# Performance work log

Measured on AMD Instinct MI355X. Metric: run time of the kernel, lower is better.

The kernel has to match this reference:

```python
import jax, jax.numpy as jnp
import numpy as np

K, A, DIM = 1024, 16384, 512


def setup_inputs() -> dict:
    key = jax.random.key(0)
    ks = jax.random.split(key, 8)
    B, H, W = 2048, 8, 8
    z_t = jax.random.randint(ks[0], (B, H, W), 0, K, dtype=jnp.int64)
    z_tp1 = jax.random.randint(ks[1], (B, H, W), 0, K, dtype=jnp.int64)
    embed_w = jax.random.normal(ks[2], (K, DIM), dtype=jnp.float32) * 0.02
    # MLP: Linear(2*dim -> dim), GELU, Linear(dim -> dim)
    lim1 = 1.0 / np.sqrt(2 * DIM)
    w1 = jax.random.uniform(ks[3], (2 * DIM, DIM), minval=-lim1, maxval=lim1, dtype=jnp.float32)
    b1 = jax.random.uniform(ks[4], (DIM,), minval=-lim1, maxval=lim1, dtype=jnp.float32)
    lim2 = 1.0 / np.sqrt(DIM)
    w2 = jax.random.uniform(ks[5], (DIM, DIM), minval=-lim2, maxval=lim2, dtype=jnp.float32)
    b2 = jax.random.uniform(ks[6], (DIM,), minval=-lim2, maxval=lim2, dtype=jnp.float32)
    codebook_w = jax.random.normal(ks[7], (A, DIM), dtype=jnp.float32) * 0.02
    return {"z_t": z_t, "z_tp1": z_tp1, "embed_w": embed_w, "w1": w1, "b1": b1,
            "w2": w2, "b2": b2, "codebook_w": codebook_w}


def reference(z_t, z_tp1, embed_w, w1, b1, w2, b2, codebook_w):
    B = z_t.shape[0]
    # embed int code grids and mean-pool over H*W tokens -> [B, dim]
    e_t = embed_w[z_t.reshape(B, -1)].mean(axis=1)
    e_tp1 = embed_w[z_tp1.reshape(B, -1)].mean(axis=1)
    h = jnp.concatenate([e_t, e_tp1], axis=-1)          # [B, 2*dim]
    h = jax.nn.gelu(h @ w1 + b1, approximate=False)
    e = h @ w2 + b2                                      # [B, dim]
    # VQ: squared L2 distance to each code, argmin, gather
    d2 = (jnp.sum(e * e, axis=1, keepdims=True)
          - 2.0 * e @ codebook_w.T
          + jnp.sum(codebook_w * codebook_w, axis=1)[None, :])  # [B, A]
    ids = jnp.argmin(d2, axis=1)                         # [B]
    q = codebook_w[ids]                                  # [B, dim]
    return ids, q
```

## Files before the change

### kernel.cpp

```cpp
#include <hip/hip_runtime.h>
#include <hip/hip_bf16.h>

#define TOK 64
#define DIMC 512

typedef __attribute__((ext_vector_type(8))) short v8s;
typedef __attribute__((ext_vector_type(4))) float v4f;

__device__ __forceinline__ unsigned int f2ord(float f) {
  unsigned int u = __float_as_uint(f);
  return (u & 0x80000000u) ? ~u : (u | 0x80000000u);
}

__device__ __forceinline__ float gelu_exact(float x) {
  return 0.5f * x * (1.0f + erff(x * 0.70710678118654752440f));
}

__device__ __forceinline__ unsigned short f2bf(float x) {
  unsigned int u = __float_as_uint(x);
  return (unsigned short)((u + 0x7FFFu + ((u >> 16) & 1u)) >> 16);
}
__device__ __forceinline__ float bf2f(unsigned short h) {
  return __uint_as_float((unsigned int)h << 16);
}

__device__ __forceinline__ void gl2lds16(const void* g, void* l) {
  __builtin_amdgcn_global_load_lds((const __attribute__((address_space(1))) void*)g,
                                   (__attribute__((address_space(3))) void*)l,
                                   16, 0, 0);
}

__global__ __launch_bounds__(256) void k_prep(
    const int* __restrict__ zt, const int* __restrict__ ztp,
    const float* __restrict__ emb,
    unsigned short* __restrict__ hh, unsigned short* __restrict__ hl,
    unsigned long long* __restrict__ rowmin,
    const float* __restrict__ w1, unsigned short* __restrict__ w1th,
    unsigned short* __restrict__ w1tl,
    const float* __restrict__ w2, unsigned short* __restrict__ w2th,
    unsigned short* __restrict__ w2tl,
    const float* __restrict__ cb, unsigned short* __restrict__ ch,
    unsigned short* __restrict__ cl, float* __restrict__ cnorm) {
  __shared__ int codes[128];
  __shared__ float tbuf[32][33];
  const int bid = blockIdx.x;
  const int tid = threadIdx.x;

  if (bid < 2048) {
    const int b = bid;
    if (tid < 64) codes[tid] = zt[b * TOK + tid];
    else if (tid < 128) codes[tid] = ztp[b * TOK + (tid - 64)];
    if (tid == 0) rowmin[b] = 0xFFFFFFFFFFFFFFFFull;
    __syncthreads();
    const int half = tid >> 7;
    const int c4 = tid & 127;
    const float4* emb4 = (const float4*)emb;
    float4 s = make_float4(0.f, 0.f, 0.f, 0.f);
    #pragma unroll 8
    for (int t = 0; t < TOK; t++) {
      const int code = codes[half * TOK + t];
      const float4 v = emb4[code * 128 + c4];
      s.x += v.x; s.y += v.y; s.z += v.z; s.w += v.w;
    }
    const float inv = 1.0f / 64.0f;
    float f[4] = {s.x * inv, s.y * inv, s.z * inv, s.w * inv};
    unsigned short hi[4], lo[4];
    #pragma unroll
    for (int i = 0; i < 4; i++) {
      hi[i] = f2bf(f[i]);
      lo[i] = f2bf(f[i] - bf2f(hi[i]));
    }
    const int off = b * 1024 + half * 512 + c4 * 4;
    *(ushort4*)&hh[off] = make_ushort4(hi[0], hi[1], hi[2], hi[3]);
    *(ushort4*)&hl[off] = make_ushort4(lo[0], lo[1], lo[2], lo[3]);
  } else if (bid < 2816) {
    const float* w; unsigned short *wth, *wtl; int Kd, N, k0, n0;
    if (bid < 2560) {
      const int i = bid - 2048;
      w = w1; wth = w1th; wtl = w1tl; Kd = 1024; N = 512;
      k0 = (i & 31) * 32; n0 = (i >> 5) * 32;
    } else {
      const int i = bid - 2560;
      w = w2; wth = w2th; wtl = w2tl; Kd = 512; N = 512;
      k0 = (i & 15) * 32; n0 = (i >> 4) * 32;
    }
    const int c = tid & 31, r = tid >> 5;
    #pragma unroll
    for (int i = 0; i < 4; i++)
      tbuf[r + i * 8][c] = w[(size_t)(k0 + r + i * 8) * N + n0 + c];
    __syncthreads();
    #pragma unroll
    for (int i = 0; i < 4; i++) {
      const float v = tbuf[c][r + i * 8];
      const unsigned short hi = f2bf(v);
      const unsigned short lo = f2bf(v - bf2f(hi));
      wth[(size_t)(n0 + r + i * 8) * Kd + k0 + c] = hi;
      wtl[(size_t)(n0 + r + i * 8) * Kd + k0 + c] = lo;
    }
  } else {
    const int row = (bid - 2816) * 4 + (tid >> 6);
    const int lane = tid & 63;
    const float4* cb4 = (const float4*)cb;
    const float4 va = cb4[row * 128 + lane * 2];
    const float4 vb = cb4[row * 128 + lane * 2 + 1];
    float s = va.x * va.x + va.y * va.y + va.z * va.z + va.w * va.w
            + vb.x * vb.x + vb.y * vb.y + vb.z * vb.z + vb.w * vb.w;
    float f[8] = {va.x, va.y, va.z, va.w, vb.x, vb.y, vb.z, vb.w};
    unsigned short hi[8], lo[8];
    #pragma unroll
    for (int i = 0; i < 8; i++) {
      hi[i] = f2bf(f[i]);
      lo[i] = f2bf(f[i] - bf2f(hi[i]));
    }
    ushort4* chp = (ushort4*)&ch[row * DIMC + lane * 8];
    ushort4* clp = (ushort4*)&cl[row * DIMC + lane * 8];
    chp[0] = make_ushort4(hi[0], hi[1], hi[2], hi[3]);
    chp[1] = make_ushort4(hi[4], hi[5], hi[6], hi[7]);
    clp[0] = make_ushort4(lo[0], lo[1], lo[2], lo[3]);
    clp[1] = make_ushort4(lo[4], lo[5], lo[6], lo[7]);
    #pragma unroll
    for (int off = 32; off > 0; off >>= 1) s += __shfl_down(s, off);
    if (lane == 0) cnorm[row] = s;
  }
}

template <bool GELU>
__global__ __launch_bounds__(256) void k_gemm(const unsigned short* __restrict__ Ah_,
                                              const unsigned short* __restrict__ Al_,
                                              const unsigned short* __restrict__ Bh_,
                                              const unsigned short* __restrict__ Bl_,
                                              const float* __restrict__ bias,
                                              unsigned short* __restrict__ oh,
                                              unsigned short* __restrict__ ol,
                                              int Kd, int N) {
  __shared__ unsigned short AhS[2][32 * 32];
  __shared__ unsigned short AlS[2][32 * 32];
  __shared__ unsigned short BhS[2][64 * 32];
  __shared__ unsigned short BlS[2][64 * 32];

  const int tid = threadIdx.x;
  const int lane = tid & 63;
  const int wid = tid >> 6;
  const int m0 = blockIdx.x * 32;
  const int n0 = blockIdx.y * 64;

  const unsigned short* Ab_h = Ah_ + (size_t)m0 * Kd;
  const unsigned short* Ab_l = Al_ + (size_t)m0 * Kd;
  const unsigned short* Bb_h = Bh_ + (size_t)n0 * Kd;
  const unsigned short* Bb_l = Bl_ + (size_t)n0 * Kd;

  const int srow = lane >> 2;
  const int sk = (lane & 3) * 8;
  const int wm = wid >> 1, wn = wid & 1;
  const int fr = lane & 15;
  const int fq = (lane >> 4) * 8;

  v4f acc[2];
  acc[0] = (v4f)(0.f);
  acc[1] = (v4f)(0.f);

  auto stage = [&](int b, int k0) {
    #pragma unroll
    for (int u = 0; u < 3; u++) {
      const int i = wid * 3 + u;
      const unsigned short* gs; unsigned short* ls; int rbase;
      if (i < 2)      { gs = Ab_h; ls = AhS[b]; rbase = i * 16; }
      else if (i < 4) { gs = Ab_l; ls = AlS[b]; rbase = (i - 2) * 16; }
      else if (i < 8) { gs = Bb_h; ls = BhS[b]; rbase = (i - 4) * 16; }
      else            { gs = Bb_l; ls = BlS[b]; rbase = (i - 8) * 16; }
      gl2lds16(gs + (size_t)(rbase + srow) * Kd + k0 + sk, ls + rbase * 32);
    }
  };

  stage(0, 0);
  int cur = 0;
  for (int k0 = 0; k0 < Kd; k0 += 32) {
    __syncthreads();
    if (k0 + 32 < Kd) stage(cur ^ 1, k0 + 32);

    const int ar = (wm * 16 + fr) * 32 + fq;
    const v8s ah = *(const v8s*)&AhS[cur][ar];
    const v8s al = *(const v8s*)&AlS[cur][ar];
    #pragma unroll
    for (int nt = 0; nt < 2; nt++) {
      const int br = (wn * 32 + nt * 16 + fr) * 32 + fq;
      const v8s bh = *(const v8s*)&BhS[cur][br];
      const v8s bl = *(const v8s*)&BlS[cur][br];
      acc[nt] = __builtin_amdgcn_mfma_f32_16x16x32_bf16(ah, bh, acc[nt], 0, 0, 0);
      acc[nt] = __builtin_amdgcn_mfma_f32_16x16x32_bf16(ah, bl, acc[nt], 0, 0, 0);
      acc[nt] = __builtin_amdgcn_mfma_f32_16x16x32_bf16(al, bh, acc[nt], 0, 0, 0);
    }
    cur ^= 1;
  }

  const int col16 = lane & 15;
  const int q = lane >> 4;
  #pragma unroll
  for (int nt = 0; nt < 2; nt++) {
    const int col = n0 + wn * 32 + nt * 16 + col16;
    const float bv = bias[col];
    #pragma unroll
    for (int reg = 0; reg < 4; reg++) {
      const int row = m0 + wm * 16 + q * 4 + reg;
      float v = acc[nt][reg] + bv;
      if (GELU) v = gelu_exact(v);
      const unsigned short hi = f2bf(v);
      oh[(size_t)row * N + col] = hi;
      ol[(size_t)row * N + col] = f2bf(v - bf2f(hi));
    }
  }
}

__global__ __launch_bounds__(256, 2) void k_vq(const unsigned short* __restrict__ eh,
                                               const unsigned short* __restrict__ el,
                                               const unsigned short* __restrict__ ch,
                                               const unsigned short* __restrict__ cl,
                                               const float* __restrict__ cnorm,
                                               unsigned long long* __restrict__ rowmin) {
  __shared__ unsigned short Ah[128 * 32];
  __shared__ unsigned short Al[128 * 32];
  __shared__ unsigned short Bh[256 * 32];
  __shared__ unsigned short Bl[256 * 32];

  const int tid = threadIdx.x;
  const int lane = tid & 63;
  const int wid = tid >> 6;
  const int bid = blockIdx.x;
  const int j = bid >> 3;
  const int x = j & 15;
  const int y = ((j >> 4) << 3) | (bid & 7);
  const int r0 = x * 128;
  const int c0 = y * 256;

  v4f acc[4][8];
  #pragma unroll
  for (int i = 0; i < 4; i++)
    #pragma unroll
    for (int jj = 0; jj < 8; jj++) acc[i][jj] = (v4f)(0.f);

  const unsigned short* ehB = eh + (size_t)r0 * DIMC;
  const unsigned short* elB = el + (size_t)r0 * DIMC;
  const unsigned short* chB = ch + (size_t)c0 * DIMC;
  const unsigned short* clB = cl + (size_t)c0 * DIMC;

  const int srow = lane >> 2;
  const int sk = (lane & 3) * 8;
  const int wm = wid >> 1;
  const int wn = wid & 1;
  const int fr = lane & 15;
  const int fq = (lane >> 4) * 8;

  for (int k0 = 0; k0 < DIMC; k0 += 32) {
    __syncthreads();
    #pragma unroll
    for (int u = 0; u < 12; u++) {
      const int i = wid * 12 + u;
      const unsigned short* gs; unsigned short* ls; int rbase;
      if (i < 8)       { gs = ehB; ls = Ah; rbase = i * 16; }
      else if (i < 16) { gs = elB; ls = Al; rbase = (i - 8) * 16; }
      else if (i < 32) { gs = chB; ls = Bh; rbase = (i - 16) * 16; }
      else             { gs = clB; ls = Bl; rbase = (i - 32) * 16; }
      gl2lds16(gs + (size_t)(rbase + srow) * DIMC + k0 + sk, ls + rbase * 32);
    }
    __syncthreads();

    v8s ahf[4], alf[4];
    #pragma unroll
    for (int mt = 0; mt < 4; mt++) {
      const int ar = (wm * 64 + mt * 16 + fr) * 32 + fq;
      ahf[mt] = *(const v8s*)&Ah[ar];
      alf[mt] = *(const v8s*)&Al[ar];
    }
    #pragma unroll
    for (int nt = 0; nt < 8; nt++) {
      const int br = (wn * 128 + nt * 16 + fr) * 32 + fq;
      const v8s bhf = *(const v8s*)&Bh[br];
      const v8s blf = *(const v8s*)&Bl[br];
      #pragma unroll
      for (int mt = 0; mt < 4; mt++) {
        acc[mt][nt] = __builtin_amdgcn_mfma_f32_16x16x32_bf16(ahf[mt], bhf, acc[mt][nt], 0, 0, 0);
        acc[mt][nt] = __builtin_amdgcn_mfma_f32_16x16x32_bf16(ahf[mt], blf, acc[mt][nt], 0, 0, 0);
        acc[mt][nt] = __builtin_amdgcn_mfma_f32_16x16x32_bf16(alf[mt], bhf, acc[mt][nt], 0, 0, 0);
      }
    }
  }

  const int col16 = lane & 15;
  const int q = lane >> 4;
  float cn[8];
  #pragma unroll
  for (int nt = 0; nt < 8; nt++) cn[nt] = cnorm[c0 + wn * 128 + nt * 16 + col16];

  #pragma unroll
  for (int mt = 0; mt < 4; mt++) {
    #pragma unroll
    for (int reg = 0; reg < 4; reg++) {
      const int row = r0 + wm * 64 + mt * 16 + q * 4 + reg;
      float best = fmaf(-2.f, acc[mt][0][reg], cn[0]);
      int bid2 = c0 + wn * 128 + col16;
      #pragma unroll
      for (int nt = 1; nt < 8; nt++) {
        const float s = fmaf(-2.f, acc[mt][nt][reg], cn[nt]);
        const int id = c0 + wn * 128 + nt * 16 + col16;
        if (s < best) { best = s; bid2 = id; }
      }
      unsigned long long v =
          ((unsigned long long)f2ord(best) << 32) | (unsigned int)bid2;
      #pragma unroll
      for (int off = 8; off > 0; off >>= 1) {
        const unsigned long long o = __shfl_down(v, off, 16);
        if (o < v) v = o;
      }
      if (col16 == 0) atomicMin(&rowmin[row], v);
    }
  }
}

__global__ __launch_bounds__(64) void k_final(const unsigned long long* __restrict__ rowmin,
                                              const float* __restrict__ cb,
                                              float* __restrict__ out,
                                              int B) {
  const int b = blockIdx.x;
  const int t = threadIdx.x;
  const unsigned long long m = rowmin[b];
  const int id = (int)(unsigned int)(m & 0xFFFFFFFFull);
  if (t == 0) out[b] = (float)id;
  float4* q4 = (float4*)(out + B) + b * 128;
  const float4* cb4 = (const float4*)cb + (size_t)id * 128;
  q4[t] = cb4[t];
  q4[t + 64] = cb4[t + 64];
}

extern "C" void kernel_launch(void* const* d_in, const int* in_sizes, int n_in,
                              void* d_out, int out_size, void* d_ws, size_t ws_size,
                              hipStream_t stream) {
  const int* zt = (const int*)d_in[0];
  const int* ztp = (const int*)d_in[1];
  const float* emb = (const float*)d_in[2];
  const float* w1 = (const float*)d_in[3];
  const float* b1 = (const float*)d_in[4];
  const float* w2 = (const float*)d_in[5];
  const float* b2 = (const float*)d_in[6];
  const float* cb = (const float*)d_in[7];
  float* out = (float*)d_out;

  const int B = in_sizes[0] / TOK;
  const int A = in_sizes[7] / DIMC;

  char* p = (char*)d_ws;
  unsigned short* hh = (unsigned short*)p;  p += (size_t)B * 1024 * 2;
  unsigned short* hl = (unsigned short*)p;  p += (size_t)B * 1024 * 2;
  unsigned short* w1th = (unsigned short*)p; p += (size_t)512 * 1024 * 2;
  unsigned short* w1tl = (unsigned short*)p; p += (size_t)512 * 1024 * 2;
  unsigned short* w2th = (unsigned short*)p; p += (size_t)512 * 512 * 2;
  unsigned short* w2tl = (unsigned short*)p; p += (size_t)512 * 512 * 2;
  unsigned short* h1h = (unsigned short*)p; p += (size_t)B * DIMC * 2;
  unsigned short* h1l = (unsigned short*)p; p += (size_t)B * DIMC * 2;
  unsigned short* eh = (unsigned short*)p;  p += (size_t)B * DIMC * 2;
  unsigned short* el = (unsigned short*)p;  p += (size_t)B * DIMC * 2;
  unsigned short* ch = (unsigned short*)p;  p += (size_t)A * DIMC * 2;
  unsigned short* cl = (unsigned short*)p;  p += (size_t)A * DIMC * 2;
  float* cnorm = (float*)p;                 p += (size_t)A * 4;
  unsigned long long* rowmin = (unsigned long long*)p;

  k_prep<<<2816 + A / 4, 256, 0, stream>>>(zt, ztp, emb, hh, hl, rowmin,
                                           w1, w1th, w1tl, w2, w2th, w2tl,
                                           cb, ch, cl, cnorm);
  k_gemm<true><<<dim3(B / 32, 512 / 64), 256, 0, stream>>>(hh, hl, w1th, w1tl, b1, h1h, h1l, 1024, 512);
  k_gemm<false><<<dim3(B / 32, 512 / 64), 256, 0, stream>>>(h1h, h1l, w2th, w2tl, b2, eh, el, 512, 512);
  k_vq<<<(B / 128) * (A / 256), 256, 0, stream>>>(eh, el, ch, cl, cnorm, rowmin);
  k_final<<<B, 64, 0, stream>>>(rowmin, cb, out, B);
}
```

Baseline: 234.6 us.

## Switch VQ distance GEMM to 32x32x16 MFMA tiles and split launch in two

The VQ kernel now uses 32x32x16 bf16 MFMA instructions with 16-float accumulators instead of 16x16x32, halving the number of fragment loads from LDS per k-step and changing the epilogue row mapping and shuffle reduction to 32-lane groups. The single 1024-block launch is split into two 512-block launches offset by a column-tile base parameter. The larger MFMA shape aims for better LDS-to-MFMA ratio; splitting the launch adds a launch boundary and may reduce tail overlap.

```diff
diff --git a/kernel.cpp b/kernel.cpp
--- a/kernel.cpp
+++ b/kernel.cpp
@@ -6,6 +6,7 @@
 
 typedef __attribute__((ext_vector_type(8))) short v8s;
 typedef __attribute__((ext_vector_type(4))) float v4f;
+typedef __attribute__((ext_vector_type(16))) float v16f;
 
 __device__ __forceinline__ unsigned int f2ord(float f) {
   unsigned int u = __float_as_uint(f);
@@ -216,7 +217,8 @@
                                                const unsigned short* __restrict__ ch,
                                                const unsigned short* __restrict__ cl,
                                                const float* __restrict__ cnorm,
-                                               unsigned long long* __restrict__ rowmin) {
+                                               unsigned long long* __restrict__ rowmin,
+                                               int y0) {
   __shared__ unsigned short Ah[128 * 32];
   __shared__ unsigned short Al[128 * 32];
   __shared__ unsigned short Bh[256 * 32];
@@ -228,15 +230,15 @@
   const int bid = blockIdx.x;
   const int j = bid >> 3;
   const int x = j & 15;
-  const int y = ((j >> 4) << 3) | (bid & 7);
+  const int y = y0 + (((j >> 4) << 3) | (bid & 7));
   const int r0 = x * 128;
   const int c0 = y * 256;
 
-  v4f acc[4][8];
+  v16f acc[2][4];
   #pragma unroll
-  for (int i = 0; i < 4; i++)
-    #pragma unroll
-    for (int jj = 0; jj < 8; jj++) acc[i][jj] = (v4f)(0.f);
+  for (int i = 0; i < 2; i++)
+    #pragma unroll
+    for (int jj = 0; jj < 4; jj++) acc[i][jj] = (v16f)(0.f);
 
   const unsigned short* ehB = eh + (size_t)r0 * DIMC;
   const unsigned short* elB = el + (size_t)r0 * DIMC;
@@ -247,8 +249,8 @@
   const int sk = (lane & 3) * 8;
   const int wm = wid >> 1;
   const int wn = wid & 1;
-  const int fr = lane & 15;
-  const int fq = (lane >> 4) * 8;
+  const int col32 = lane & 31;
+  const int khalf = lane >> 5;
 
   for (int k0 = 0; k0 < DIMC; k0 += 32) {
     __syncthreads();
@@ -264,54 +266,56 @@
     }
     __syncthreads();
 
-    v8s ahf[4], alf[4];
-    #pragma unroll
-    for (int mt = 0; mt < 4; mt++) {
-      const int ar = (wm * 64 + mt * 16 + fr) * 32 + fq;
-      ahf[mt] = *(const v8s*)&Ah[ar];
-      alf[mt] = *(const v8s*)&Al[ar];
-    }
-    #pragma unroll
-    for (int nt = 0; nt < 8; nt++) {
-      const int br = (wn * 128 + nt * 16 + fr) * 32 + fq;
-      const v8s bhf = *(const v8s*)&Bh[br];
-      const v8s blf = *(const v8s*)&Bl[br];
+    #pragma unroll
+    for (int sub = 0; sub < 2; sub++) {
+      const int ko = sub * 16 + khalf * 8;
+      v8s ahf[2], alf[2];
       #pragma unroll
-      for (int mt = 0; mt < 4; mt++) {
-        acc[mt][nt] = __builtin_amdgcn_mfma_f32_16x16x32_bf16(ahf[mt], bhf, acc[mt][nt], 0, 0, 0);
-        acc[mt][nt] = __builtin_amdgcn_mfma_f32_16x16x32_bf16(ahf[mt], blf, acc[mt][nt], 0, 0, 0);
-        acc[mt][nt] = __builtin_amdgcn_mfma_f32_16x16x32_bf16(alf[mt], bhf, acc[mt][nt], 0, 0, 0);
+      for (int mt = 0; mt < 2; mt++) {
+        const int ar = (wm * 64 + mt * 32 + col32) * 32 + ko;
+        ahf[mt] = *(const v8s*)&Ah[ar];
+        alf[mt] = *(const v8s*)&Al[ar];
       }
-    }
-  }
-
-  const int col16 = lane & 15;
-  const int q = lane >> 4;
-  float cn[8];
+      #pragma unroll
+      for (int nt = 0; nt < 4; nt++) {
+        const int br = (wn * 128 + nt * 32 + col32) * 32 + ko;
+        const v8s bhf = *(const v8s*)&Bh[br];
+        const v8s blf = *(const v8s*)&Bl[br];
+        #pragma unroll
+        for (int mt = 0; mt < 2; mt++) {
+          acc[mt][nt] = __builtin_amdgcn_mfma_f32_32x32x16_bf16(ahf[mt], bhf, acc[mt][nt], 0, 0, 0);
+          acc[mt][nt] = __builtin_amdgcn_mfma_f32_32x32x16_bf16(ahf[mt], blf, acc[mt][nt], 0, 0, 0);
+          acc[mt][nt] = __builtin_amdgcn_mfma_f32_32x32x16_bf16(alf[mt], bhf, acc[mt][nt], 0, 0, 0);
+        }
+      }
+    }
+  }
+
+  float cn[4];
   #pragma unroll
-  for (int nt = 0; nt < 8; nt++) cn[nt] = cnorm[c0 + wn * 128 + nt * 16 + col16];
+  for (int nt = 0; nt < 4; nt++) cn[nt] = cnorm[c0 + wn * 128 + nt * 32 + col32];
 
   #pragma unroll
-  for (int mt = 0; mt < 4; mt++) {
-    #pragma unroll
-    for (int reg = 0; reg < 4; reg++) {
-      const int row = r0 + wm * 64 + mt * 16 + q * 4 + reg;
+  for (int mt = 0; mt < 2; mt++) {
+    #pragma unroll
+    for (int reg = 0; reg < 16; reg++) {
+      const int row = r0 + wm * 64 + mt * 32 + (reg & 3) + 8 * (reg >> 2) + 4 * khalf;
       float best = fmaf(-2.f, acc[mt][0][reg], cn[0]);
-      int bid2 = c0 + wn * 128 + col16;
+      int bid2 = c0 + wn * 128 + col32;
       #pragma unroll
-      for (int nt = 1; nt < 8; nt++) {
+      for (int nt = 1; nt < 4; nt++) {
         const float s = fmaf(-2.f, acc[mt][nt][reg], cn[nt]);
-        const int id = c0 + wn * 128 + nt * 16 + col16;
+        const int id = c0 + wn * 128 + nt * 32 + col32;
         if (s < best) { best = s; bid2 = id; }
       }
       unsigned long long v =
           ((unsigned long long)f2ord(best) << 32) | (unsigned int)bid2;
       #pragma unroll
-      for (int off = 8; off > 0; off >>= 1) {
-        const unsigned long long o = __shfl_down(v, off, 16);
+      for (int off = 16; off > 0; off >>= 1) {
+        const unsigned long long o = __shfl_down(v, off, 32);
         if (o < v) v = o;
       }
-      if (col16 == 0) atomicMin(&rowmin[row], v);
+      if (col32 == 0) atomicMin(&rowmin[row], v);
     }
   }
 }
@@ -368,6 +372,7 @@
                                            cb, ch, cl, cnorm);
   k_gemm<true><<<dim3(B / 32, 512 / 64), 256, 0, stream>>>(hh, hl, w1th, w1tl, b1, h1h, h1l, 1024, 512);
   k_gemm<false><<<dim3(B / 32, 512 / 64), 256, 0, stream>>>(h1h, h1l, w2th, w2tl, b2, eh, el, 512, 512);
-  k_vq<<<(B / 128) * (A / 256), 256, 0, stream>>>(eh, el, ch, cl, cnorm, rowmin);
+  k_vq<<<512, 256, 0, stream>>>(eh, el, ch, cl, cnorm, rowmin, 0);
+  k_vq<<<512, 256, 0, stream>>>(eh, el, ch, cl, cnorm, rowmin, 32);
   k_final<<<B, 64, 0, stream>>>(rowmin, cb, out, B);
 }
```

Result: slower. 257.3 us (+9.7%).

## Double-buffer VQ GEMM LDS tiles and shrink codebook tile to 128

Applied to the files above, without the earlier changes.

Splits the VQ distance kernel's shared-memory tiles into two buffers so that the global-to-LDS loads for the next K-slice are issued while MFMAs run on the current one, with one barrier per iteration. The codebook tile per block drops from 256 to 128 columns, halving the accumulators and doubling the grid. This aims to hide load latency and ease register pressure. The cost is lower data reuse per block, twice as many per-row atomicMin reductions, and more LDS per block.

```diff
diff --git a/kernel.cpp b/kernel.cpp
--- a/kernel.cpp
+++ b/kernel.cpp
@@ -29,6 +29,7 @@
                                    (__attribute__((address_space(3))) void*)l,
                                    16, 0, 0);
 }
+
 
 __global__ __launch_bounds__(256) void k_prep(
     const int* __restrict__ zt, const int* __restrict__ ztp,
@@ -217,10 +218,10 @@
                                                const unsigned short* __restrict__ cl,
                                                const float* __restrict__ cnorm,
                                                unsigned long long* __restrict__ rowmin) {
-  __shared__ unsigned short Ah[128 * 32];
-  __shared__ unsigned short Al[128 * 32];
-  __shared__ unsigned short Bh[256 * 32];
-  __shared__ unsigned short Bl[256 * 32];
+  __shared__ unsigned short AhS[2][128 * 32];
+  __shared__ unsigned short AlS[2][128 * 32];
+  __shared__ unsigned short BhS[2][128 * 32];
+  __shared__ unsigned short BlS[2][128 * 32];
 
   const int tid = threadIdx.x;
   const int lane = tid & 63;
@@ -230,13 +231,13 @@
   const int x = j & 15;
   const int y = ((j >> 4) << 3) | (bid & 7);
   const int r0 = x * 128;
-  const int c0 = y * 256;
-
-  v4f acc[4][8];
+  const int c0 = y * 128;
+
+  v4f acc[4][4];
   #pragma unroll
   for (int i = 0; i < 4; i++)
     #pragma unroll
-    for (int jj = 0; jj < 8; jj++) acc[i][jj] = (v4f)(0.f);
+    for (int jj = 0; jj < 4; jj++) acc[i][jj] = (v4f)(0.f);
 
   const unsigned short* ehB = eh + (size_t)r0 * DIMC;
   const unsigned short* elB = el + (size_t)r0 * DIMC;
@@ -250,32 +251,37 @@
   const int fr = lane & 15;
   const int fq = (lane >> 4) * 8;
 
+  auto stage = [&](int b, int k0) {
+    #pragma unroll
+    for (int u = 0; u < 8; u++) {
+      const int i = wid * 8 + u;
+      const unsigned short* gs; unsigned short* ls; int rbase;
+      if (i < 8)       { gs = ehB; ls = AhS[b]; rbase = i * 16; }
+      else if (i < 16) { gs = elB; ls = AlS[b]; rbase = (i - 8) * 16; }
+      else if (i < 24) { gs = chB; ls = BhS[b]; rbase = (i - 16) * 16; }
+      else             { gs = clB; ls = BlS[b]; rbase = (i - 24) * 16; }
+      gl2lds16(gs + (size_t)(rbase + srow) * DIMC + k0 + sk, ls + rbase * 32);
+    }
+  };
+
+  stage(0, 0);
+  int cur = 0;
   for (int k0 = 0; k0 < DIMC; k0 += 32) {
     __syncthreads();
-    #pragma unroll
-    for (int u = 0; u < 12; u++) {
-      const int i = wid * 12 + u;
-      const unsigned short* gs; unsigned short* ls; int rbase;
-      if (i < 8)       { gs = ehB; ls = Ah; rbase = i * 16; }
-      else if (i < 16) { gs = elB; ls = Al; rbase = (i - 8) * 16; }
-      else if (i < 32) { gs = chB; ls = Bh; rbase = (i - 16) * 16; }
-      else             { gs = clB; ls = Bl; rbase = (i - 32) * 16; }
-      gl2lds16(gs + (size_t)(rbase + srow) * DIMC + k0 + sk, ls + rbase * 32);
-    }
-    __syncthreads();
+    if (k0 + 32 < DIMC) stage(cur ^ 1, k0 + 32);
 
     v8s ahf[4], alf[4];
     #pragma unroll
     for (int mt = 0; mt < 4; mt++) {
       const int ar = (wm * 64 + mt * 16 + fr) * 32 + fq;
-      ahf[mt] = *(const v8s*)&Ah[ar];
-      alf[mt] = *(const v8s*)&Al[ar];
-    }
-    #pragma unroll
-    for (int nt = 0; nt < 8; nt++) {
-      const int br = (wn * 128 + nt * 16 + fr) * 32 + fq;
-      const v8s bhf = *(const v8s*)&Bh[br];
-      const v8s blf = *(const v8s*)&Bl[br];
+      ahf[mt] = *(const v8s*)&AhS[cur][ar];
+      alf[mt] = *(const v8s*)&AlS[cur][ar];
+    }
+    #pragma unroll
+    for (int nt = 0; nt < 4; nt++) {
+      const int br = (wn * 64 + nt * 16 + fr) * 32 + fq;
+      const v8s bhf = *(const v8s*)&BhS[cur][br];
+      const v8s blf = *(const v8s*)&BlS[cur][br];
       #pragma unroll
       for (int mt = 0; mt < 4; mt++) {
         acc[mt][nt] = __builtin_amdgcn_mfma_f32_16x16x32_bf16(ahf[mt], bhf, acc[mt][nt], 0, 0, 0);
@@ -283,13 +289,14 @@
         acc[mt][nt] = __builtin_amdgcn_mfma_f32_16x16x32_bf16(alf[mt], bhf, acc[mt][nt], 0, 0, 0);
       }
     }
+    cur ^= 1;
   }
 
   const int col16 = lane & 15;
   const int q = lane >> 4;
-  float cn[8];
+  float cn[4];
   #pragma unroll
-  for (int nt = 0; nt < 8; nt++) cn[nt] = cnorm[c0 + wn * 128 + nt * 16 + col16];
+  for (int nt = 0; nt < 4; nt++) cn[nt] = cnorm[c0 + wn * 64 + nt * 16 + col16];
 
   #pragma unroll
   for (int mt = 0; mt < 4; mt++) {
@@ -297,11 +304,11 @@
     for (int reg = 0; reg < 4; reg++) {
       const int row = r0 + wm * 64 + mt * 16 + q * 4 + reg;
       float best = fmaf(-2.f, acc[mt][0][reg], cn[0]);
-      int bid2 = c0 + wn * 128 + col16;
+      int bid2 = c0 + wn * 64 + col16;
       #pragma unroll
-      for (int nt = 1; nt < 8; nt++) {
+      for (int nt = 1; nt < 4; nt++) {
         const float s = fmaf(-2.f, acc[mt][nt][reg], cn[nt]);
-        const int id = c0 + wn * 128 + nt * 16 + col16;
+        const int id = c0 + wn * 64 + nt * 16 + col16;
         if (s < best) { best = s; bid2 = id; }
       }
       unsigned long long v =
@@ -368,6 +375,6 @@
                                            cb, ch, cl, cnorm);
   k_gemm<true><<<dim3(B / 32, 512 / 64), 256, 0, stream>>>(hh, hl, w1th, w1tl, b1, h1h, h1l, 1024, 512);
   k_gemm<false><<<dim3(B / 32, 512 / 64), 256, 0, stream>>>(h1h, h1l, w2th, w2tl, b2, eh, el, 512, 512);
-  k_vq<<<(B / 128) * (A / 256), 256, 0, stream>>>(eh, el, ch, cl, cnorm, rowmin);
+  k_vq<<<(B / 128) * (A / 128), 256, 0, stream>>>(eh, el, ch, cl, cnorm, rowmin);
   k_final<<<B, 64, 0, stream>>>(rowmin, cb, out, B);
 }
```

Result: slower. 245.4 us (+4.6%).
